# Kernel optimization log

Measured on AMD Instinct MI355X. Metric: run time of the kernel, lower is better.

Reference implementation:

```python
import jax, jax.numpy as jnp
import numpy as np

SIGMA = 2.0
INF = 1.0e6
M, N, H, K, C_IN, C_OUT = 50000, 100000, 32, 15, 64, 64
RADIUS = 2.5


def setup_inputs() -> dict:
    key = jax.random.key(0)
    k1, k2, k3, k4, k5, k6 = jax.random.split(key, 6)
    q_points = jax.random.normal(k1, (M, 3), dtype=jnp.float32)
    s_points = jax.random.normal(k2, (N, 3), dtype=jnp.float32)
    s_feats = jax.random.normal(k3, (N, C_IN), dtype=jnp.float32)
    # index N refers to the padding point (placed at INF)
    neighbor_indices = jax.random.randint(k4, (M, H), 0, N + 1, dtype=jnp.int64)
    weights = jax.random.normal(k5, (K, C_IN, C_OUT), dtype=jnp.float32) * 0.05
    # kernel points inside sphere of RADIUS (stand-in for load_kernels buffer)
    kp = jax.random.normal(k6, (K, 3), dtype=jnp.float32)
    kp = kp / jnp.linalg.norm(kp, axis=1, keepdims=True) * RADIUS * 0.7
    kernel_points = kp.at[0].set(0.0)  # fixed='center'
    return {
        "q_points": q_points,
        "s_points": s_points,
        "s_feats": s_feats,
        "neighbor_indices": neighbor_indices,
        "weights": weights,
        "kernel_points": kernel_points,
    }


def reference(q_points, s_points, s_feats, neighbor_indices, weights, kernel_points):
    # pad support points with an 'infinity' shadow point at index N
    padded_pts = jnp.concatenate([s_points, jnp.full((1, 3), INF, s_points.dtype)], axis=0)
    neighbors = padded_pts[neighbor_indices]                    # (M, H, 3)
    rel = neighbors - q_points[:, None, :]                      # (M, H, 3)
    diff = rel[:, :, None, :] - kernel_points[None, None]       # (M, H, K, 3)
    sq_dist = jnp.sum(diff * diff, axis=-1)                     # (M, H, K)
    nbr_w = jnp.clip(1.0 - jnp.sqrt(sq_dist) / SIGMA, 0.0)      # (M, H, K)

    padded_feats = jnp.concatenate([s_feats, jnp.zeros((1, s_feats.shape[1]), s_feats.dtype)], axis=0)
    nbr_feats = padded_feats[neighbor_indices]                  # (M, H, C_in)

    weighted = jnp.einsum('mhk,mhc->mkc', nbr_w, nbr_feats)     # (M, K, C_in)
    out = jnp.einsum('mkc,kcd->md', weighted, weights)          # (M, C_out)

    # normalize by count of real (non-padding / nonzero-sum) neighbors
    nbr_sum = jnp.sum(nbr_feats, axis=-1)                       # (M, H)
    nbr_num = jnp.sum(nbr_sum > 0.0, axis=-1)                   # (M,)
    nbr_num = jnp.maximum(nbr_num, 1)
    return out / nbr_num[:, None].astype(out.dtype)
```

## Files before the change

### kernel.cpp

```cpp
#include <hip/hip_runtime.h>
#include <hip/hip_bf16.h>

#define MPTS 50000
#define NPTS 100000
#define KK 15
#define TM 16
#define WTP 1036
#define STP 36

typedef __attribute__((ext_vector_type(8))) short short8;
typedef __attribute__((ext_vector_type(4))) short short4v;
typedef __attribute__((ext_vector_type(4))) float floatx4;

static __device__ __forceinline__ unsigned short f2bf(float f) {
    __hip_bfloat16 h = __float2bfloat16(f);
    return *reinterpret_cast<unsigned short*>(&h);
}

static __device__ __forceinline__ short8 lds_load8(const unsigned short* p) {
    const short4v a = *(const short4v*)p;
    const short4v b = *(const short4v*)(p + 4);
    short8 r;
    r[0] = a[0]; r[1] = a[1]; r[2] = a[2]; r[3] = a[3];
    r[4] = b[0]; r[5] = b[1]; r[6] = b[2]; r[7] = b[3];
    return r;
}

__global__ void prep_all(const float* __restrict__ sf, const float* __restrict__ w,
                         const float* __restrict__ kpts,
                         unsigned short* __restrict__ sfb, float* __restrict__ rs,
                         unsigned short* __restrict__ wbf2, float4* __restrict__ kpp) {
    const int b = blockIdx.x, t = threadIdx.x;
    if (b < 782) {
        const int tt = b * 256 + t;
        const int row = tt >> 1, p = tt & 1;
        if (row < NPTS) {
            const float* base = sf + (size_t)row * 64 + p * 4;
            float4 r = *(const float4*)base;
            {
                ushort4 o;
                o.x = f2bf(r.x); o.y = f2bf(r.y); o.z = f2bf(r.z); o.w = f2bf(r.w);
                *(ushort4*)&sfb[(size_t)row * 64 + p * 4] = o;
            }
#pragma unroll
            for (int i = 1; i < 8; i++) {
                const float4 x = *(const float4*)(base + i * 8);
                ushort4 o;
                o.x = f2bf(x.x); o.y = f2bf(x.y); o.z = f2bf(x.z); o.w = f2bf(x.w);
                *(ushort4*)&sfb[(size_t)row * 64 + i * 8 + p * 4] = o;
                r.x += x.x; r.y += x.y; r.z += x.z; r.w += x.w;
            }
            float sp = (r.x + r.y) + (r.z + r.w);
            sp += __shfl_xor(sp, 1);
            if (p == 0) rs[row] = sp;
        }
    } else if (b < 814) {
        const int e = (b - 782) * 256 + t;
        const int lane = e & 63, s = (e >> 6) & 31, wq = e >> 11;
        const int d = wq * 16 + (lane & 15);
        const int lqp = lane >> 4;
        unsigned short o8[8];
#pragma unroll
        for (int j = 0; j < 8; j++) {
            const int kc = s * 32 + lqp * 8 + j;
            const int c = kc >> 4, k = kc & 15;
            o8[j] = (k < KK) ? f2bf(w[k * 4096 + c * 64 + d]) : (unsigned short)0;
        }
#pragma unroll
        for (int j = 0; j < 8; j++) wbf2[(size_t)e * 8 + j] = o8[j];
    } else {
        if (t < 16) *(ushort4*)&sfb[(size_t)NPTS * 64 + t * 4] = make_ushort4(0, 0, 0, 0);
        else if (t == 16) rs[NPTS] = -1.0f;
        else if (t >= 32 && t < 32 + KK) {
            const int k = t - 32;
            const float kx = kpts[k * 3 + 0], ky = kpts[k * 3 + 1], kz = kpts[k * 3 + 2];
            kpp[k] = make_float4(-2.f * kx, -2.f * ky, -2.f * kz, kx * kx + ky * ky + kz * kz);
        }
    }
}

__global__ __launch_bounds__(512, 4) void kpconv_fused(
    const float* __restrict__ q_points,
    const float* __restrict__ s_points,
    const unsigned short* __restrict__ sfb,
    const int*   __restrict__ nbr,
    const unsigned short* __restrict__ wbf2,
    const float4* __restrict__ kpp,
    const float* __restrict__ rowsum,
    float* __restrict__ out)
{
    const int t    = threadIdx.x;
    const int m0   = blockIdx.x * TM;
    const int lane = t & 63;
    const int wv   = t >> 6;
    const int l15  = lane & 15;
    const int lq   = lane >> 4;

    __shared__ int idx_lds[TM][32];
    __shared__ __align__(16) unsigned short stage[8][64 * STP];
    __shared__ unsigned short wtw[TM * WTP];
    __shared__ float inv_lds[TM];

    const int mw = 2 * wv + (lane >> 5);
    const int h  = lane & 31;
    idx_lds[mw][h] = nbr[(size_t)(m0 + mw) * 32 + h];

    const int idxp = idx_lds[mw][h];
    float px = 1.0e6f, py = 1.0e6f, pz = 1.0e6f;
    if (idxp < NPTS) {
        px = s_points[idxp * 3 + 0];
        py = s_points[idxp * 3 + 1];
        pz = s_points[idxp * 3 + 2];
    }

    ushort4 g[2][8];
    const int c4 = l15 * 4;
#pragma unroll
    for (int mi = 0; mi < 2; mi++) {
        const int m = 2 * wv + mi;
#pragma unroll
        for (int g2 = 0; g2 < 4; g2++) {
            const int r0 = g2 * 8 + lq * 2;
            const int2 ip = *(const int2*)&idx_lds[m][r0];
            const int i0 = min(ip.x, NPTS);
            const int i1 = min(ip.y, NPTS);
            g[mi][2 * g2]     = *(const ushort4*)&sfb[(size_t)i0 * 64 + c4];
            g[mi][2 * g2 + 1] = *(const ushort4*)&sfb[(size_t)i1 * 64 + c4];
        }
    }

    {
        const float rx = px - q_points[(m0 + mw) * 3 + 0];
        const float ry = py - q_points[(m0 + mw) * 3 + 1];
        const float rz = pz - q_points[(m0 + mw) * 3 + 2];
        const float r2 = rx * rx + ry * ry + rz * rz;
        unsigned short* wrow = &wtw[mw * WTP];
#pragma unroll
        for (int k = 0; k < KK; k++) {
            const float4 kp = kpp[k];
            float d2 = kp.w;
            d2 = fmaf(rx, kp.x, d2);
            d2 = fmaf(ry, kp.y, d2);
            d2 = fmaf(rz, kp.z, d2);
            d2 = fmaxf(r2 + d2, 0.0f);
            const float wv_ = fmaxf(fmaf(-0.5f, __builtin_amdgcn_sqrtf(d2), 1.0f), 0.0f);
            wrow[k * STP + h] = f2bf(wv_);
        }
        wrow[15 * STP + h] = 0;

        const bool ok = rowsum[min(idxp, NPTS)] > 0.0f;
        const unsigned long long bal = __ballot(ok);
        if (h == 0) {
            const int cnt = __popc((unsigned)(bal >> ((lane >> 5) * 32)));
            inv_lds[mw] = 1.0f / (float)(cnt < 1 ? 1 : cnt);
        }
    }

    unsigned short* const st = stage[wv];
    const int swzw = (l15 >> 2) << 2;
#pragma unroll
    for (int mi = 0; mi < 2; mi++) {
        const int m = 2 * wv + mi;

#pragma unroll
        for (int g2 = 0; g2 < 4; g2++) {
            const int so = ((g2 * 4 + lq) ^ swzw) * 2;
            const ushort4 a = g[mi][2 * g2];
            const ushort4 b = g[mi][2 * g2 + 1];
            *(unsigned*)&st[(c4 + 0) * STP + so] = (unsigned)a.x | ((unsigned)b.x << 16);
            *(unsigned*)&st[(c4 + 1) * STP + so] = (unsigned)a.y | ((unsigned)b.y << 16);
            *(unsigned*)&st[(c4 + 2) * STP + so] = (unsigned)a.z | ((unsigned)b.z << 16);
            *(unsigned*)&st[(c4 + 3) * STP + so] = (unsigned)a.w | ((unsigned)b.w << 16);
        }

        const short8 afrag = lds_load8(&wtw[m * WTP + l15 * STP + lq * 8]);
#pragma unroll
        for (int ct = 0; ct < 4; ct++) {
            const short8 bfrag = lds_load8(&st[(ct * 16 + l15) * STP + ((lq ^ ct) * 8)]);
            floatx4 d = {0.f, 0.f, 0.f, 0.f};
            d = __builtin_amdgcn_mfma_f32_16x16x32_bf16(afrag, bfrag, d, 0, 0, 0);
            ushort4 pk;
            pk.x = f2bf(d[0]); pk.y = f2bf(d[1]); pk.z = f2bf(d[2]); pk.w = f2bf(d[3]);
            *(ushort4*)&wtw[m * WTP + (ct * 16 + l15) * 16 + lq * 4] = pk;
        }
    }
    __syncthreads();

    {
        const int q  = wv & 3;
        const int kh = wv >> 2;
        floatx4 acc = {0.f, 0.f, 0.f, 0.f};
        const unsigned short* ap = &wtw[l15 * WTP + kh * 512 + lq * 8];
        const unsigned short* bp = wbf2 + ((size_t)((q * 32 + kh * 16) * 64) + lane) * 8;
#pragma unroll 8
        for (int s = 0; s < 16; s++) {
            const short8 a = lds_load8(ap + s * 32);
            const short8 b = *(const short8*)(bp + s * 512);
            acc = __builtin_amdgcn_mfma_f32_16x16x32_bf16(a, b, acc, 0, 0, 0);
        }

        float* const scratch = (float*)&stage[0][0];
        if (kh == 1) {
            *(floatx4*)&scratch[q * 256 + l15 * 16 + lq * 4] = acc;
        }
        __syncthreads();
        if (kh == 0) {
            const floatx4 p = *(const floatx4*)&scratch[q * 256 + l15 * 16 + lq * 4];
            const int d = q * 16 + l15;
#pragma unroll
            for (int r = 0; r < 4; r++) {
                const int m = lq * 4 + r;
                out[(size_t)(m0 + m) * 64 + d] = (acc[r] + p[r]) * inv_lds[m];
            }
        }
    }
}

extern "C" void kernel_launch(void* const* d_in, const int* in_sizes, int n_in,
                              void* d_out, int out_size, void* d_ws, size_t ws_size,
                              hipStream_t stream) {
    const float* q_points = (const float*)d_in[0];
    const float* s_points = (const float*)d_in[1];
    const float* s_feats  = (const float*)d_in[2];
    const int*   nbr      = (const int*)d_in[3];
    const float* weights  = (const float*)d_in[4];
    const float* kpts     = (const float*)d_in[5];
    float* out = (float*)d_out;

    char* ws = (char*)d_ws;
    unsigned short* wbf2 = (unsigned short*)ws;
    float* rowsum = (float*)(ws + 131072);
    float4* kpp = (float4*)(ws + 531600);
    unsigned short* sfb = (unsigned short*)(ws + 532480);

    prep_all<<<815, 256, 0, stream>>>(s_feats, weights, kpts, sfb, rowsum, wbf2, kpp);
    kpconv_fused<<<MPTS / TM, 512, 0, stream>>>(q_points, s_points, sfb, nbr,
                                                wbf2, kpp, rowsum, out);
}
```

Measured before the change: 142.2 us.

## Shrink LDS footprint with half-width staging to raise blocks per CU

Drops the LDS index buffer and reads neighbor indices straight from global memory. It halves the per-wave feature staging tile by splitting the 32-neighbor contraction into two 16-neighbor passes, each an MFMA with a zero-masked A fragment accumulated into registers. It also tightens the wtw row pitch and raises the launch-bounds occupancy hint from 4 to 6, aiming for more resident blocks per CU to hide gather latency. The cost is double the MFMAs in that stage, extra accumulator registers under a tighter register budget, and redundant global index loads.

```diff
diff --git a/kernel.cpp b/kernel.cpp
--- a/kernel.cpp
+++ b/kernel.cpp
@@ -5,8 +5,9 @@
 #define NPTS 100000
 #define KK 15
 #define TM 16
-#define WTP 1036
+#define WTP 1028
 #define STP 36
+#define STPH 20
 
 typedef __attribute__((ext_vector_type(8))) short short8;
 typedef __attribute__((ext_vector_type(4))) short short4v;
@@ -79,7 +80,7 @@
     }
 }
 
-__global__ __launch_bounds__(512, 4) void kpconv_fused(
+__global__ __launch_bounds__(512, 6) void kpconv_fused(
     const float* __restrict__ q_points,
     const float* __restrict__ s_points,
     const unsigned short* __restrict__ sfb,
@@ -96,16 +97,15 @@
     const int l15  = lane & 15;
     const int lq   = lane >> 4;
 
-    __shared__ int idx_lds[TM][32];
-    __shared__ __align__(16) unsigned short stage[8][64 * STP];
+    __shared__ __align__(16) unsigned short stage[8][64 * STPH];
     __shared__ unsigned short wtw[TM * WTP];
     __shared__ float inv_lds[TM];
 
     const int mw = 2 * wv + (lane >> 5);
     const int h  = lane & 31;
-    idx_lds[mw][h] = nbr[(size_t)(m0 + mw) * 32 + h];
-
-    const int idxp = idx_lds[mw][h];
+
+    const int idxp = nbr[(size_t)(m0 + mw) * 32 + h];
+
     float px = 1.0e6f, py = 1.0e6f, pz = 1.0e6f;
     if (idxp < NPTS) {
         px = s_points[idxp * 3 + 0];
@@ -121,7 +121,7 @@
 #pragma unroll
         for (int g2 = 0; g2 < 4; g2++) {
             const int r0 = g2 * 8 + lq * 2;
-            const int2 ip = *(const int2*)&idx_lds[m][r0];
+            const int2 ip = *(const int2*)&nbr[(size_t)(m0 + m) * 32 + r0];
             const int i0 = min(ip.x, NPTS);
             const int i1 = min(ip.y, NPTS);
             g[mi][2 * g2]     = *(const ushort4*)&sfb[(size_t)i0 * 64 + c4];
@@ -157,30 +157,45 @@
     }
 
     unsigned short* const st = stage[wv];
-    const int swzw = (l15 >> 2) << 2;
+    const int swzh = (l15 >> 3) << 2;
+    const short8 zero8 = {0, 0, 0, 0, 0, 0, 0, 0};
 #pragma unroll
     for (int mi = 0; mi < 2; mi++) {
         const int m = 2 * wv + mi;
 
-#pragma unroll
-        for (int g2 = 0; g2 < 4; g2++) {
-            const int so = ((g2 * 4 + lq) ^ swzw) * 2;
-            const ushort4 a = g[mi][2 * g2];
-            const ushort4 b = g[mi][2 * g2 + 1];
-            *(unsigned*)&st[(c4 + 0) * STP + so] = (unsigned)a.x | ((unsigned)b.x << 16);
-            *(unsigned*)&st[(c4 + 1) * STP + so] = (unsigned)a.y | ((unsigned)b.y << 16);
-            *(unsigned*)&st[(c4 + 2) * STP + so] = (unsigned)a.z | ((unsigned)b.z << 16);
-            *(unsigned*)&st[(c4 + 3) * STP + so] = (unsigned)a.w | ((unsigned)b.w << 16);
-        }
-
-        const short8 afrag = lds_load8(&wtw[m * WTP + l15 * STP + lq * 8]);
+        const short8 afull = lds_load8(&wtw[m * WTP + l15 * STP + lq * 8]);
+
+        floatx4 d[4];
+#pragma unroll
+        for (int ct = 0; ct < 4; ct++) d[ct] = (floatx4){0.f, 0.f, 0.f, 0.f};
+
+#pragma unroll
+        for (int r = 0; r < 2; r++) {
+#pragma unroll
+            for (int g2h = 0; g2h < 2; g2h++) {
+                const int g2 = 2 * r + g2h;
+                const int so = (((g2h * 4 + lq) ^ swzh)) * 2;
+                const ushort4 a = g[mi][2 * g2];
+                const ushort4 b = g[mi][2 * g2 + 1];
+                *(unsigned*)&st[(c4 + 0) * STPH + so] = (unsigned)a.x | ((unsigned)b.x << 16);
+                *(unsigned*)&st[(c4 + 1) * STPH + so] = (unsigned)a.y | ((unsigned)b.y << 16);
+                *(unsigned*)&st[(c4 + 2) * STPH + so] = (unsigned)a.z | ((unsigned)b.z << 16);
+                *(unsigned*)&st[(c4 + 3) * STPH + so] = (unsigned)a.w | ((unsigned)b.w << 16);
+            }
+            const short8 ar = ((lq >> 1) == r) ? afull : zero8;
+#pragma unroll
+            for (int ct = 0; ct < 4; ct++) {
+                const short8 bfrag =
+                    lds_load8(&st[(ct * 16 + l15) * STPH + (((lq & 1) ^ (ct >> 1)) * 8)]);
+                d[ct] = __builtin_amdgcn_mfma_f32_16x16x32_bf16(ar, bfrag, d[ct], 0, 0, 0);
+            }
+        }
+
 #pragma unroll
         for (int ct = 0; ct < 4; ct++) {
-            const short8 bfrag = lds_load8(&st[(ct * 16 + l15) * STP + ((lq ^ ct) * 8)]);
-            floatx4 d = {0.f, 0.f, 0.f, 0.f};
-            d = __builtin_amdgcn_mfma_f32_16x16x32_bf16(afrag, bfrag, d, 0, 0, 0);
             ushort4 pk;
-            pk.x = f2bf(d[0]); pk.y = f2bf(d[1]); pk.z = f2bf(d[2]); pk.w = f2bf(d[3]);
+            pk.x = f2bf(d[ct][0]); pk.y = f2bf(d[ct][1]);
+            pk.z = f2bf(d[ct][2]); pk.w = f2bf(d[ct][3]);
             *(ushort4*)&wtw[m * WTP + (ct * 16 + l15) * 16 + lq * 4] = pk;
         }
     }
@@ -188,7 +203,7 @@
 
     {
         const int q  = wv & 3;
-        const int kh = wv >> 2;
+        const int kh = wv >> 1 >> 1;
         floatx4 acc = {0.f, 0.f, 0.f, 0.f};
         const unsigned short* ap = &wtw[l15 * WTP + kh * 512 + lq * 8];
         const unsigned short* bp = wbf2 + ((size_t)((q * 32 + kh * 16) * 64) + lane) * 8;
```

After: 142.4 us. About the same (+0.1%).

## Make fused kernel persistent with register-cached weights and packed point records

Applied to the files above, without the earlier changes.

Turns the main kernel into a persistent grid of 512 blocks that loops over point tiles. Each wave loads its slice of the bf16 weight matrix into registers once instead of re-reading it for every tile. Support point coordinates and the nonzero-row-sum flag are packed into one float4 per point in the prep kernel, so each neighbor needs a single gather instead of separate position and row-sum loads, and neighbor indices are read from global memory directly rather than staged in LDS. The trade-offs are 16 short8 registers per thread, which may limit occupancy under the 512x4 launch bound, and fewer blocks to hide gather latency.

```diff
diff --git a/kernel.cpp b/kernel.cpp
--- a/kernel.cpp
+++ b/kernel.cpp
@@ -5,7 +5,9 @@
 #define NPTS 100000
 #define KK 15
 #define TM 16
-#define WTP 1036
+#define NTILES (MPTS / TM)
+#define PGRID 512
+#define WTP 1028
 #define STP 36
 
 typedef __attribute__((ext_vector_type(8))) short short8;
@@ -27,8 +29,8 @@
 }
 
 __global__ void prep_all(const float* __restrict__ sf, const float* __restrict__ w,
-                         const float* __restrict__ kpts,
-                         unsigned short* __restrict__ sfb, float* __restrict__ rs,
+                         const float* __restrict__ kpts, const float* __restrict__ spt,
+                         unsigned short* __restrict__ sfb, float4* __restrict__ spts4,
                          unsigned short* __restrict__ wbf2, float4* __restrict__ kpp) {
     const int b = blockIdx.x, t = threadIdx.x;
     if (b < 782) {
@@ -52,7 +54,10 @@
             }
             float sp = (r.x + r.y) + (r.z + r.w);
             sp += __shfl_xor(sp, 1);
-            if (p == 0) rs[row] = sp;
+            if (p == 0) {
+                spts4[row] = make_float4(spt[row * 3 + 0], spt[row * 3 + 1],
+                                         spt[row * 3 + 2], sp > 0.0f ? 1.0f : -1.0f);
+            }
         }
     } else if (b < 814) {
         const int e = (b - 782) * 256 + t;
@@ -70,7 +75,7 @@
         for (int j = 0; j < 8; j++) wbf2[(size_t)e * 8 + j] = o8[j];
     } else {
         if (t < 16) *(ushort4*)&sfb[(size_t)NPTS * 64 + t * 4] = make_ushort4(0, 0, 0, 0);
-        else if (t == 16) rs[NPTS] = -1.0f;
+        else if (t == 16) spts4[NPTS] = make_float4(1.0e6f, 1.0e6f, 1.0e6f, -1.0f);
         else if (t >= 32 && t < 32 + KK) {
             const int k = t - 32;
             const float kx = kpts[k * 3 + 0], ky = kpts[k * 3 + 1], kz = kpts[k * 3 + 2];
@@ -81,136 +86,141 @@
 
 __global__ __launch_bounds__(512, 4) void kpconv_fused(
     const float* __restrict__ q_points,
-    const float* __restrict__ s_points,
+    const float4* __restrict__ spts4,
     const unsigned short* __restrict__ sfb,
     const int*   __restrict__ nbr,
     const unsigned short* __restrict__ wbf2,
     const float4* __restrict__ kpp,
-    const float* __restrict__ rowsum,
     float* __restrict__ out)
 {
     const int t    = threadIdx.x;
-    const int m0   = blockIdx.x * TM;
     const int lane = t & 63;
     const int wv   = t >> 6;
     const int l15  = lane & 15;
     const int lq   = lane >> 4;
 
-    __shared__ int idx_lds[TM][32];
     __shared__ __align__(16) unsigned short stage[8][64 * STP];
     __shared__ unsigned short wtw[TM * WTP];
     __shared__ float inv_lds[TM];
+    __shared__ __align__(16) float scratch[1024];
 
     const int mw = 2 * wv + (lane >> 5);
     const int h  = lane & 31;
-    idx_lds[mw][h] = nbr[(size_t)(m0 + mw) * 32 + h];
-
-    const int idxp = idx_lds[mw][h];
-    float px = 1.0e6f, py = 1.0e6f, pz = 1.0e6f;
-    if (idxp < NPTS) {
-        px = s_points[idxp * 3 + 0];
-        py = s_points[idxp * 3 + 1];
-        pz = s_points[idxp * 3 + 2];
-    }
-
-    ushort4 g[2][8];
     const int c4 = l15 * 4;
-#pragma unroll
-    for (int mi = 0; mi < 2; mi++) {
-        const int m = 2 * wv + mi;
-#pragma unroll
-        for (int g2 = 0; g2 < 4; g2++) {
-            const int r0 = g2 * 8 + lq * 2;
-            const int2 ip = *(const int2*)&idx_lds[m][r0];
-            const int i0 = min(ip.x, NPTS);
-            const int i1 = min(ip.y, NPTS);
-            g[mi][2 * g2]     = *(const ushort4*)&sfb[(size_t)i0 * 64 + c4];
-            g[mi][2 * g2 + 1] = *(const ushort4*)&sfb[(size_t)i1 * 64 + c4];
-        }
-    }
-
+
+    const int q  = wv & 3;
+    const int kh = wv >> 2;
+    const unsigned short* const ap = &wtw[l15 * WTP + kh * 512 + lq * 8];
+
+    short8 wf[16];
     {
-        const float rx = px - q_points[(m0 + mw) * 3 + 0];
-        const float ry = py - q_points[(m0 + mw) * 3 + 1];
-        const float rz = pz - q_points[(m0 + mw) * 3 + 2];
-        const float r2 = rx * rx + ry * ry + rz * rz;
-        unsigned short* wrow = &wtw[mw * WTP];
-#pragma unroll
-        for (int k = 0; k < KK; k++) {
-            const float4 kp = kpp[k];
-            float d2 = kp.w;
-            d2 = fmaf(rx, kp.x, d2);
-            d2 = fmaf(ry, kp.y, d2);
-            d2 = fmaf(rz, kp.z, d2);
-            d2 = fmaxf(r2 + d2, 0.0f);
-            const float wv_ = fmaxf(fmaf(-0.5f, __builtin_amdgcn_sqrtf(d2), 1.0f), 0.0f);
-            wrow[k * STP + h] = f2bf(wv_);
-        }
-        wrow[15 * STP + h] = 0;
-
-        const bool ok = rowsum[min(idxp, NPTS)] > 0.0f;
-        const unsigned long long bal = __ballot(ok);
-        if (h == 0) {
-            const int cnt = __popc((unsigned)(bal >> ((lane >> 5) * 32)));
-            inv_lds[mw] = 1.0f / (float)(cnt < 1 ? 1 : cnt);
-        }
+        const unsigned short* const bp =
+            wbf2 + ((size_t)((q * 32 + kh * 16) * 64) + lane) * 8;
+#pragma unroll
+        for (int s = 0; s < 16; s++) wf[s] = *(const short8*)(bp + s * 512);
     }
 
     unsigned short* const st = stage[wv];
     const int swzw = (l15 >> 2) << 2;
-#pragma unroll
-    for (int mi = 0; mi < 2; mi++) {
-        const int m = 2 * wv + mi;
-
-#pragma unroll
-        for (int g2 = 0; g2 < 4; g2++) {
-            const int so = ((g2 * 4 + lq) ^ swzw) * 2;
-            const ushort4 a = g[mi][2 * g2];
-            const ushort4 b = g[mi][2 * g2 + 1];
-            *(unsigned*)&st[(c4 + 0) * STP + so] = (unsigned)a.x | ((unsigned)b.x << 16);
-            *(unsigned*)&st[(c4 + 1) * STP + so] = (unsigned)a.y | ((unsigned)b.y << 16);
-            *(unsigned*)&st[(c4 + 2) * STP + so] = (unsigned)a.z | ((unsigned)b.z << 16);
-            *(unsigned*)&st[(c4 + 3) * STP + so] = (unsigned)a.w | ((unsigned)b.w << 16);
-        }
-
-        const short8 afrag = lds_load8(&wtw[m * WTP + l15 * STP + lq * 8]);
-#pragma unroll
-        for (int ct = 0; ct < 4; ct++) {
-            const short8 bfrag = lds_load8(&st[(ct * 16 + l15) * STP + ((lq ^ ct) * 8)]);
-            floatx4 d = {0.f, 0.f, 0.f, 0.f};
-            d = __builtin_amdgcn_mfma_f32_16x16x32_bf16(afrag, bfrag, d, 0, 0, 0);
-            ushort4 pk;
-            pk.x = f2bf(d[0]); pk.y = f2bf(d[1]); pk.z = f2bf(d[2]); pk.w = f2bf(d[3]);
-            *(ushort4*)&wtw[m * WTP + (ct * 16 + l15) * 16 + lq * 4] = pk;
-        }
-    }
-    __syncthreads();
-
-    {
-        const int q  = wv & 3;
-        const int kh = wv >> 2;
-        floatx4 acc = {0.f, 0.f, 0.f, 0.f};
-        const unsigned short* ap = &wtw[l15 * WTP + kh * 512 + lq * 8];
-        const unsigned short* bp = wbf2 + ((size_t)((q * 32 + kh * 16) * 64) + lane) * 8;
-#pragma unroll 8
-        for (int s = 0; s < 16; s++) {
-            const short8 a = lds_load8(ap + s * 32);
-            const short8 b = *(const short8*)(bp + s * 512);
-            acc = __builtin_amdgcn_mfma_f32_16x16x32_bf16(a, b, acc, 0, 0, 0);
-        }
-
-        float* const scratch = (float*)&stage[0][0];
-        if (kh == 1) {
-            *(floatx4*)&scratch[q * 256 + l15 * 16 + lq * 4] = acc;
+
+    for (int tile = blockIdx.x; tile < NTILES; tile += PGRID) {
+        const int m0 = tile * TM;
+
+        const int idxp = nbr[(size_t)(m0 + mw) * 32 + h];
+        const float4 sp4 = spts4[min(idxp, NPTS)];
+        ushort4 g[2][8];
+#pragma unroll
+        for (int mi = 0; mi < 2; mi++) {
+            const int m = 2 * wv + mi;
+#pragma unroll
+            for (int g2 = 0; g2 < 4; g2++) {
+                const int r0 = g2 * 8 + lq * 2;
+                const int2 ip = *(const int2*)&nbr[(size_t)(m0 + m) * 32 + r0];
+                const int i0 = min(ip.x, NPTS);
+                const int i1 = min(ip.y, NPTS);
+                g[mi][2 * g2]     = *(const ushort4*)&sfb[(size_t)i0 * 64 + c4];
+                g[mi][2 * g2 + 1] = *(const ushort4*)&sfb[(size_t)i1 * 64 + c4];
+            }
+        }
+
+        {
+            const float rx = sp4.x - q_points[(m0 + mw) * 3 + 0];
+            const float ry = sp4.y - q_points[(m0 + mw) * 3 + 1];
+            const float rz = sp4.z - q_points[(m0 + mw) * 3 + 2];
+            const float r2 = rx * rx + ry * ry + rz * rz;
+            unsigned short* wrow = &wtw[mw * WTP];
+#pragma unroll
+            for (int k = 0; k < KK; k++) {
+                const float4 kp = kpp[k];
+                float d2 = kp.w;
+                d2 = fmaf(rx, kp.x, d2);
+                d2 = fmaf(ry, kp.y, d2);
+                d2 = fmaf(rz, kp.z, d2);
+                d2 = fmaxf(r2 + d2, 0.0f);
+                const float wv_ = fmaxf(fmaf(-0.5f, __builtin_amdgcn_sqrtf(d2), 1.0f), 0.0f);
+                wrow[k * STP + h] = f2bf(wv_);
+            }
+            wrow[15 * STP + h] = 0;
+
+            const unsigned long long bal = __ballot(sp4.w > 0.0f);
+            if (h == 0) {
+                const int cnt = __popc((unsigned)(bal >> ((lane >> 5) * 32)));
+                inv_lds[mw] = 1.0f / (float)(cnt < 1 ? 1 : cnt);
+            }
+        }
+
+#pragma unroll
+        for (int mi = 0; mi < 2; mi++) {
+            const int m = 2 * wv + mi;
+
+#pragma unroll
+            for (int g2 = 0; g2 < 4; g2++) {
+                const int so = ((g2 * 4 + lq) ^ swzw) * 2;
+                const ushort4 a = g[mi][2 * g2];
+                const ushort4 b = g[mi][2 * g2 + 1];
+                *(unsigned*)&st[(c4 + 0) * STP + so] = (unsigned)a.x | ((unsigned)b.x << 16);
+                *(unsigned*)&st[(c4 + 1) * STP + so] = (unsigned)a.y | ((unsigned)b.y << 16);
+                *(unsigned*)&st[(c4 + 2) * STP + so] = (unsigned)a.z | ((unsigned)b.z << 16);
+                *(unsigned*)&st[(c4 + 3) * STP + so] = (unsigned)a.w | ((unsigned)b.w << 16);
+            }
+
+            const short8 afrag = lds_load8(&wtw[m * WTP + l15 * STP + lq * 8]);
+#pragma unroll
+            for (int ct = 0; ct < 4; ct++) {
+                const short8 bfrag = lds_load8(&st[(ct * 16 + l15) * STP + ((lq ^ ct) * 8)]);
+                floatx4 d = {0.f, 0.f, 0.f, 0.f};
+                d = __builtin_amdgcn_mfma_f32_16x16x32_bf16(afrag, bfrag, d, 0, 0, 0);
+                ushort4 pk;
+                pk.x = f2bf(d[0]); pk.y = f2bf(d[1]); pk.z = f2bf(d[2]); pk.w = f2bf(d[3]);
+                *(ushort4*)&wtw[m * WTP + (ct * 16 + l15) * 16 + lq * 4] = pk;
+            }
         }
         __syncthreads();
-        if (kh == 0) {
-            const floatx4 p = *(const floatx4*)&scratch[q * 256 + l15 * 16 + lq * 4];
-            const int d = q * 16 + l15;
-#pragma unroll
-            for (int r = 0; r < 4; r++) {
-                const int m = lq * 4 + r;
-                out[(size_t)(m0 + m) * 64 + d] = (acc[r] + p[r]) * inv_lds[m];
+
+        {
+            float inv4[4];
+            if (kh == 0) {
+#pragma unroll
+                for (int r = 0; r < 4; r++) inv4[r] = inv_lds[lq * 4 + r];
+            }
+            floatx4 acc = {0.f, 0.f, 0.f, 0.f};
+#pragma unroll
+            for (int s = 0; s < 16; s++) {
+                const short8 a = lds_load8(ap + s * 32);
+                acc = __builtin_amdgcn_mfma_f32_16x16x32_bf16(a, wf[s], acc, 0, 0, 0);
+            }
+            if (kh == 1) {
+                *(floatx4*)&scratch[q * 256 + l15 * 16 + lq * 4] = acc;
+            }
+            __syncthreads();
+            if (kh == 0) {
+                const floatx4 p = *(const floatx4*)&scratch[q * 256 + l15 * 16 + lq * 4];
+                const int d = q * 16 + l15;
+#pragma unroll
+                for (int r = 0; r < 4; r++) {
+                    const int m = lq * 4 + r;
+                    out[(size_t)(m0 + m) * 64 + d] = (acc[r] + p[r]) * inv4[r];
+                }
             }
         }
     }
@@ -229,11 +239,12 @@
 
     char* ws = (char*)d_ws;
     unsigned short* wbf2 = (unsigned short*)ws;
-    float* rowsum = (float*)(ws + 131072);
-    float4* kpp = (float4*)(ws + 531600);
-    unsigned short* sfb = (unsigned short*)(ws + 532480);
-
-    prep_all<<<815, 256, 0, stream>>>(s_feats, weights, kpts, sfb, rowsum, wbf2, kpp);
-    kpconv_fused<<<MPTS / TM, 512, 0, stream>>>(q_points, s_points, sfb, nbr,
-                                                wbf2, kpp, rowsum, out);
-}
+    float4* spts4 = (float4*)(ws + 131072);
+    float4* kpp = (float4*)(ws + 1731088);
+    unsigned short* sfb = (unsigned short*)(ws + 1731584);
+
+    prep_all<<<815, 256, 0, stream>>>(s_feats, weights, kpts, s_points,
+                                      sfb, spts4, wbf2, kpp);
+    kpconv_fused<<<PGRID, 512, 0, stream>>>(q_points, spts4, sfb, nbr,
+                                            wbf2, kpp, out);
+}
```

Result: slower. 163.5 us (+15.0%).
